# Optimization experiments

Measured on AMD Instinct MI355X. Metric: run time of the kernel, lower is better.

The kernel has to match this reference:

```python
import jax, jax.numpy as jnp
import numpy as np

B, NLOC, F, H = 16384, 12, 512, 256

def setup_inputs() -> dict:
    key = jax.random.key(0)
    ks = jax.random.split(key, 8)
    s = lambda n: 1.0 / np.sqrt(n)
    return {
        "global_feature": jax.random.normal(ks[0], (B, F), jnp.float32),
        "local_features": jax.random.normal(ks[1], (B, NLOC, F), jnp.float32),
        "Wq": jax.random.normal(ks[2], (F, H), jnp.float32) * s(F),
        "bq": jnp.zeros((H,), jnp.float32),
        "Wk": jax.random.normal(ks[3], (F, H), jnp.float32) * s(F),
        "bk": jnp.zeros((H,), jnp.float32),
        "Wv": jax.random.normal(ks[4], (F, H), jnp.float32) * s(F),
        "bv": jnp.zeros((H,), jnp.float32),
        "w_dr": jax.random.normal(ks[5], (NLOC,), jnp.float32) * s(NLOC),  # Linear(12,1) weight
        "b_dr": jnp.zeros((), jnp.float32),
        "Wf": jax.random.normal(ks[6], (2 * H, F), jnp.float32) * s(2 * H),
        "bf": jnp.zeros((F,), jnp.float32),
    }

def reference(global_feature, local_features, Wq, bq, Wk, bk, Wv, bv, w_dr, b_dr, Wf, bf):
    scale = 1.0 / jnp.sqrt(jnp.float32(H))
    # dimension_reduction over the 12 local tokens: Linear(12 -> 1)
    lf_mean = jnp.einsum('bkf,k->bf', local_features, w_dr) + b_dr  # [B, F]
    # --- local queries attend to the single global token ---
    gk = global_feature @ Wk + bk                       # [B, H]
    gv = global_feature @ Wv + bv                       # [B, H]
    lq = local_features @ Wq + bq                       # [B, 12, H]
    s1 = (jnp.einsum('bkh,bh->bk', lq, gk) * scale)[..., None]  # [B, 12, 1]
    a1 = jax.nn.softmax(s1, axis=-1)                    # softmax over length-1 key axis
    weighted_global = a1 * gv[:, None, :]               # [B, 12, H]
    # --- global query attends over the 12 local tokens ---
    gq = global_feature @ Wq + bq                       # [B, H]
    lk = local_features @ Wk + bk                       # [B, 12, H]
    lv = local_features @ Wv + bv                       # [B, 12, H]
    s2 = jnp.einsum('bh,bkh->bk', gq, lk) * scale       # [B, 12]
    a2 = jax.nn.softmax(s2, axis=-1)
    local_to_global = jnp.einsum('bk,bkh->bh', a2, lv)  # [B, H]
    # pool the 12-token axis of the weighted global feature
    wg_mean = jnp.einsum('bkh,k->bh', weighted_global, w_dr) + b_dr  # [B, H]
    combined = jnp.concatenate([local_to_global, wg_mean], axis=-1)  # [B, 2H]
    fused = jax.nn.relu(combined @ Wf + bf) + lf_mean + global_feature  # [B, F]
    return fused
```

## Files before the change

### kernel.cpp

```cpp
#include <hip/hip_runtime.h>

#define NLOC 12
#define F_DIM 512
#define H_DIM 256

typedef float f4 __attribute__((ext_vector_type(4)));
typedef _Float16 half4 __attribute__((ext_vector_type(4)));
typedef _Float16 half8 __attribute__((ext_vector_type(8)));

#define OFF_W1   0ul
#define OFF_W2   (OFF_W1 + 512ul*512*2)
#define OFF_C1   (OFF_W2 + 512ul*1024*2)
#define OFF_CVEC (OFF_C1 + 2048ul)
#define OFF_ACAT (OFF_CVEC + 2048ul)
#define OFF_BASE (OFF_ACAT + 16384ul*1024*2)

__global__ void __launch_bounds__(256) precompute_w(
    const float* __restrict__ Wq, const float* __restrict__ Wk,
    const float* __restrict__ Wv, const float* __restrict__ Wf,
    const float* __restrict__ wdr,
    _Float16* __restrict__ W1, _Float16* __restrict__ W2)
{
    __shared__ float X[32][264];
    __shared__ float Y[32][264];
    const int mode = blockIdx.z;
    const int f0 = blockIdx.x * 32;
    const int j0 = blockIdx.y * 32;
    const int t = threadIdx.x;

    {
        const int r = t >> 3, cb = (t & 7) * 32;
        const float* ysrc = ((mode == 0) ? Wq : Wv) + (j0 + r) * H_DIM + cb;
#pragma unroll
        for (int u = 0; u < 32; u += 4)
            *(f4*)&Y[r][cb + u] = *(const f4*)(ysrc + u);
        if (mode == 0) {
            const float* xsrc = Wk + (f0 + r) * H_DIM + cb;
#pragma unroll
            for (int u = 0; u < 32; u += 4)
                *(f4*)&X[r][cb + u] = *(const f4*)(xsrc + u);
        }
    }
    if (mode != 0) {
        const int h = t;
        const int hoff = (mode == 2) ? H_DIM : 0;
        const float* xsrc = Wf + (long)(h + hoff) * F_DIM + f0;
        f4 v[8];
#pragma unroll
        for (int u = 0; u < 8; ++u) v[u] = *(const f4*)(xsrc + u * 4);
#pragma unroll
        for (int r = 0; r < 32; ++r) X[r][h] = v[r >> 2][r & 3];
    }
    __syncthreads();

    const int fy = t >> 4, jx = t & 15;
    float a00 = 0.f, a01 = 0.f, a10 = 0.f, a11 = 0.f;
#pragma unroll 8
    for (int h = 0; h < H_DIM; ++h) {
        float x0 = X[fy][h], x1 = X[fy + 16][h];
        float y0 = Y[jx][h], y1 = Y[jx + 16][h];
        a00 += x0 * y0; a01 += x0 * y1; a10 += x1 * y0; a11 += x1 * y1;
    }
    if (mode == 2) {
        float S = 0.f;
#pragma unroll
        for (int k = 0; k < NLOC; ++k) S += wdr[k];
        a00 *= S; a01 *= S; a10 *= S; a11 *= S;
    }
    if (mode == 0) {
        W1[(f0 + fy) * F_DIM + (j0 + jx)]             = (_Float16)a00;
        W1[(f0 + fy) * F_DIM + (j0 + jx + 16)]        = (_Float16)a01;
        W1[(f0 + fy + 16) * F_DIM + (j0 + jx)]        = (_Float16)a10;
        W1[(f0 + fy + 16) * F_DIM + (j0 + jx + 16)]   = (_Float16)a11;
    } else {
        const long co = (mode == 2) ? F_DIM : 0;
        W2[(long)(f0 + fy) * 1024 + co + (j0 + jx)]           = (_Float16)a00;
        W2[(long)(f0 + fy) * 1024 + co + (j0 + jx + 16)]      = (_Float16)a01;
        W2[(long)(f0 + fy + 16) * 1024 + co + (j0 + jx)]      = (_Float16)a10;
        W2[(long)(f0 + fy + 16) * 1024 + co + (j0 + jx + 16)] = (_Float16)a11;
    }
}

__global__ void __launch_bounds__(256) cvec_kernel(
    const float* __restrict__ Wk, const float* __restrict__ Wf,
    const float* __restrict__ bq, const float* __restrict__ bv,
    const float* __restrict__ wdr, const float* __restrict__ bdr,
    const float* __restrict__ bfv,
    float* __restrict__ c1, float* __restrict__ cvec)
{
    const int f = blockIdx.x * 256 + threadIdx.x;
    f4 a = {0.f, 0.f, 0.f, 0.f};
    const f4* wk4 = (const f4*)(Wk + (long)f * H_DIM);
    const f4* bq4 = (const f4*)bq;
#pragma unroll 4
    for (int h4 = 0; h4 < H_DIM / 4; ++h4) a += wk4[h4] * bq4[h4];
    c1[f] = a[0] + a[1] + a[2] + a[3];

    float s1 = 0.f, s2 = 0.f, s3 = 0.f;
#pragma unroll 4
    for (int h = 0; h < H_DIM; ++h) {
        float w1v = Wf[h * F_DIM + f];
        float w2v = Wf[(H_DIM + h) * F_DIM + f];
        float bvh = bv[h];
        s1 += bvh * w1v; s2 += bvh * w2v; s3 += w2v;
    }
    float S = 0.f;
#pragma unroll
    for (int k = 0; k < NLOC; ++k) S += wdr[k];
    cvec[f] = s1 + S * s2 + bdr[0] * s3 + bfv[f];
}

__global__ void __launch_bounds__(256, 2) fused_local(
    const float* __restrict__ g, const float* __restrict__ loc,
    const _Float16* __restrict__ W1, const float* __restrict__ c1,
    const float* __restrict__ wdr, const float* __restrict__ bdr,
    _Float16* __restrict__ Acat, _Float16* __restrict__ base)
{
    __shared__ _Float16 G[32][520];
    __shared__ _Float16 T[32][520];
    const int tid = threadIdx.x;
    const int lane = tid & 63;
    const int wave = tid >> 6;
    const int quad = lane >> 4;
    const int l16 = lane & 15;
    const long m0 = (long)blockIdx.x * 32;

    {
        const int r = tid >> 3;
        const int cb = (tid & 7) * 8;
#pragma unroll
        for (int u = 0; u < 512; u += 64) {
            const float* src = g + (m0 + r) * F_DIM + cb + u;
            f4 v0 = *(const f4*)(src);
            f4 v1 = *(const f4*)(src + 4);
            half8 hv;
#pragma unroll
            for (int j = 0; j < 4; ++j) { hv[j] = (_Float16)v0[j]; hv[4 + j] = (_Float16)v1[j]; }
            *(half8*)&G[r][cb + u] = hv;
            *(half8*)(Acat + (m0 + r) * 1024 + 512 + cb + u) = hv;
        }
    }
    __syncthreads();

    const int wn1 = wave * 32;
    for (int nt = 0; nt < 4; ++nt) {
        const int n0 = nt * 128;
        const _Float16* wb0 = W1 + (long)(n0 + wn1 + l16) * F_DIM + quad * 8;
        const _Float16* wb1 = wb0 + 16 * F_DIM;
        f4 acc[2][2] = {{{0.f,0.f,0.f,0.f},{0.f,0.f,0.f,0.f}},
                        {{0.f,0.f,0.f,0.f},{0.f,0.f,0.f,0.f}}};
#pragma unroll
        for (int k0 = 0; k0 < 512; k0 += 32) {
            half8 b0 = *(const half8*)(wb0 + k0);
            half8 b1 = *(const half8*)(wb1 + k0);
            half8 a0 = *(const half8*)&G[l16][k0 + quad * 8];
            half8 a1 = *(const half8*)&G[16 + l16][k0 + quad * 8];
            acc[0][0] = __builtin_amdgcn_mfma_f32_16x16x32_f16(a0, b0, acc[0][0], 0, 0, 0);
            acc[0][1] = __builtin_amdgcn_mfma_f32_16x16x32_f16(a0, b1, acc[0][1], 0, 0, 0);
            acc[1][0] = __builtin_amdgcn_mfma_f32_16x16x32_f16(a1, b0, acc[1][0], 0, 0, 0);
            acc[1][1] = __builtin_amdgcn_mfma_f32_16x16x32_f16(a1, b1, acc[1][1], 0, 0, 0);
        }
#pragma unroll
        for (int ni = 0; ni < 2; ++ni) {
            const int col = n0 + wn1 + ni * 16 + l16;
            const float cv = c1[col];
#pragma unroll
            for (int mi = 0; mi < 2; ++mi)
#pragma unroll
                for (int i = 0; i < 4; ++i)
                    T[mi * 16 + quad * 4 + i][col] = (_Float16)(acc[mi][ni][i] + cv);
        }
    }
    __syncthreads();

    const int c0 = lane * 4;
    const int c1i = 256 + lane * 4;
    const float bd = bdr[0];
    float wv[NLOC];
#pragma unroll
    for (int k = 0; k < NLOC; ++k) wv[k] = wdr[k];

    for (int rr = 0; rr < 8; ++rr) {
        const int bl = wave * 8 + rr;
        const long b = m0 + bl;
        const float* lb = loc + b * (NLOC * F_DIM);

        f4 la[NLOC], lbv[NLOC];
#pragma unroll
        for (int k = 0; k < NLOC; ++k) {
            la[k]  = *(const f4*)(lb + k * F_DIM + c0);
            lbv[k] = *(const f4*)(lb + k * F_DIM + c1i);
        }
        f4 taf = __builtin_convertvector(*(const half4*)&T[bl][c0], f4);
        f4 tbf = __builtin_convertvector(*(const half4*)&T[bl][c1i], f4);

        float p[NLOC];
#pragma unroll
        for (int k = 0; k < NLOC; ++k) {
            f4 prod = la[k] * taf + lbv[k] * tbf;
            p[k] = prod[0] + prod[1] + prod[2] + prod[3];
        }
#pragma unroll
        for (int k = 0; k < NLOC; ++k) {
            float v = p[k];
            v += __shfl_xor(v, 1);
            v += __shfl_xor(v, 2);
            v += __shfl_xor(v, 4);
            v += __shfl_xor(v, 8);
            v += __shfl_xor(v, 16);
            v += __shfl_xor(v, 32);
            p[k] = v * 0.0625f;
        }
        float mx = p[0];
#pragma unroll
        for (int k = 1; k < NLOC; ++k) mx = fmaxf(mx, p[k]);
        float e[NLOC], s = 0.f;
#pragma unroll
        for (int k = 0; k < NLOC; ++k) { e[k] = expf(p[k] - mx); s += e[k]; }
        const float inv = 1.f / s;

        f4 pA = {0.f,0.f,0.f,0.f}, pB = {0.f,0.f,0.f,0.f};
        f4 fA = {0.f,0.f,0.f,0.f}, fB = {0.f,0.f,0.f,0.f};
#pragma unroll
        for (int k = 0; k < NLOC; ++k) {
            const float ak = e[k] * inv;
            const float wk = wv[k];
            pA += ak * la[k]; pB += ak * lbv[k];
            fA += wk * la[k]; fB += wk * lbv[k];
        }
        half4 gA = *(const half4*)&G[bl][c0];
        half4 gB = *(const half4*)&G[bl][c1i];
        fA += bd + __builtin_convertvector(gA, f4);
        fB += bd + __builtin_convertvector(gB, f4);

        *(half4*)(Acat + b * 1024 + c0)          = __builtin_convertvector(pA, half4);
        *(half4*)(Acat + b * 1024 + c1i)         = __builtin_convertvector(pB, half4);
        *(half4*)(base + b * F_DIM + c0)         = __builtin_convertvector(fA, half4);
        *(half4*)(base + b * F_DIM + c1i)        = __builtin_convertvector(fB, half4);
    }
}

__global__ void __launch_bounds__(256, 3) gemm_final(
    const _Float16* __restrict__ A, const _Float16* __restrict__ Bt,
    const float* __restrict__ cvec, const _Float16* __restrict__ base,
    float* __restrict__ out)
{
    __shared__ _Float16 As[2][64][40];
    const int tid = threadIdx.x;
    const int lane = tid & 63;
    const int wave = tid >> 6;
    const int quad = lane >> 4;
    const int l16 = lane & 15;
    const int wm = (wave & 1) * 32;
    const int wn = (wave >> 1) * 64;
    const long m0 = (long)blockIdx.x * 64;
    const int n0 = blockIdx.y * 128;
    const int srA = tid >> 2, scA = (tid & 3) * 8;

    const _Float16* bp0 = Bt + (long)(n0 + wn + l16) * 1024 + quad * 8;
    const _Float16* bp1 = bp0 + 16 * 1024;
    const _Float16* bp2 = bp0 + 32 * 1024;
    const _Float16* bp3 = bp0 + 48 * 1024;
    const _Float16* ap  = A + (m0 + srA) * 1024 + scA;

    f4 acc[2][4];
#pragma unroll
    for (int mi = 0; mi < 2; ++mi)
#pragma unroll
        for (int nj = 0; nj < 4; ++nj) acc[mi][nj] = (f4){0.f,0.f,0.f,0.f};

    *(uint4*)&As[0][srA][scA] = *(const uint4*)(ap);
    __syncthreads();

#pragma unroll
    for (int kt = 0; kt < 32; ++kt) {
        const int k0 = kt * 32;
        uint4 avn;
        if (kt < 31) avn = *(const uint4*)(ap + k0 + 32);
        half8 b0 = *(const half8*)(bp0 + k0);
        half8 b1 = *(const half8*)(bp1 + k0);
        half8 b2 = *(const half8*)(bp2 + k0);
        half8 b3 = *(const half8*)(bp3 + k0);
        half8 a0 = *(const half8*)&As[kt & 1][wm + l16][quad * 8];
        half8 a1 = *(const half8*)&As[kt & 1][wm + 16 + l16][quad * 8];
        acc[0][0] = __builtin_amdgcn_mfma_f32_16x16x32_f16(a0, b0, acc[0][0], 0, 0, 0);
        acc[1][0] = __builtin_amdgcn_mfma_f32_16x16x32_f16(a1, b0, acc[1][0], 0, 0, 0);
        acc[0][1] = __builtin_amdgcn_mfma_f32_16x16x32_f16(a0, b1, acc[0][1], 0, 0, 0);
        acc[1][1] = __builtin_amdgcn_mfma_f32_16x16x32_f16(a1, b1, acc[1][1], 0, 0, 0);
        acc[0][2] = __builtin_amdgcn_mfma_f32_16x16x32_f16(a0, b2, acc[0][2], 0, 0, 0);
        acc[1][2] = __builtin_amdgcn_mfma_f32_16x16x32_f16(a1, b2, acc[1][2], 0, 0, 0);
        acc[0][3] = __builtin_amdgcn_mfma_f32_16x16x32_f16(a0, b3, acc[0][3], 0, 0, 0);
        acc[1][3] = __builtin_amdgcn_mfma_f32_16x16x32_f16(a1, b3, acc[1][3], 0, 0, 0);
        if (kt < 31) *(uint4*)&As[(kt & 1) ^ 1][srA][scA] = avn;
        __syncthreads();
    }

#pragma unroll
    for (int mi = 0; mi < 2; ++mi)
#pragma unroll
        for (int nj = 0; nj < 4; ++nj) {
            const int col = n0 + wn + nj * 16 + l16;
            const float cv = cvec[col];
#pragma unroll
            for (int i = 0; i < 4; ++i) {
                const long row = m0 + wm + mi * 16 + quad * 4 + i;
                float v = acc[mi][nj][i] + cv;
                v = fmaxf(v, 0.f) + (float)base[row * F_DIM + col];
                out[row * F_DIM + col] = v;
            }
        }
}

extern "C" void kernel_launch(void* const* d_in, const int* in_sizes, int n_in,
                              void* d_out, int out_size, void* d_ws, size_t ws_size,
                              hipStream_t stream)
{
    (void)in_sizes; (void)n_in; (void)out_size; (void)ws_size;
    const float* gf  = (const float*)d_in[0];
    const float* loc = (const float*)d_in[1];
    const float* Wq  = (const float*)d_in[2];
    const float* bq  = (const float*)d_in[3];
    const float* Wk  = (const float*)d_in[4];
    const float* Wv  = (const float*)d_in[6];
    const float* bv  = (const float*)d_in[7];
    const float* wdr = (const float*)d_in[8];
    const float* bdr = (const float*)d_in[9];
    const float* Wf  = (const float*)d_in[10];
    const float* bfv = (const float*)d_in[11];
    float* out = (float*)d_out;

    char* ws = (char*)d_ws;
    _Float16* W1   = (_Float16*)(ws + OFF_W1);
    _Float16* W2   = (_Float16*)(ws + OFF_W2);
    float*    c1   = (float*)(ws + OFF_C1);
    float*    cvec = (float*)(ws + OFF_CVEC);
    _Float16* Acat = (_Float16*)(ws + OFF_ACAT);
    _Float16* base = (_Float16*)(ws + OFF_BASE);

    precompute_w<<<dim3(16, 16, 3), 256, 0, stream>>>(Wq, Wk, Wv, Wf, wdr, W1, W2);
    cvec_kernel<<<2, 256, 0, stream>>>(Wk, Wf, bq, bv, wdr, bdr, bfv, c1, cvec);
    fused_local<<<512, 256, 0, stream>>>(gf, loc, W1, c1, wdr, bdr, Acat, base);
    gemm_final<<<dim3(256, 4), 256, 0, stream>>>(Acat, W2, cvec, base, out);
}
```

Baseline: 719.7 us.

## Enlarge final GEMM tile with LDS-staged B, prefetch local rows, merge cvec kernel

The final GEMM moves from 64x128 to 128x128 block tiles. Both A and B are now staged through double-buffered shared memory, and each wave computes a 4x4 grid of MFMA tiles, which raises reuse and cuts redundant global B loads. The fused_local kernel now software-pipelines the next row's first half of local features during the current row's compute, and its barrier moves after the first prefetch. The cvec kernel is folded into precompute_w as an extra grid slice to save one launch. The larger tile uses more registers and LDS, so launch bounds drop to 2 blocks per SM and grid-level parallelism is halved.

```diff
diff --git a/kernel.cpp b/kernel.cpp
--- a/kernel.cpp
+++ b/kernel.cpp
@@ -18,15 +18,44 @@
 __global__ void __launch_bounds__(256) precompute_w(
     const float* __restrict__ Wq, const float* __restrict__ Wk,
     const float* __restrict__ Wv, const float* __restrict__ Wf,
-    const float* __restrict__ wdr,
-    _Float16* __restrict__ W1, _Float16* __restrict__ W2)
+    const float* __restrict__ wdr, const float* __restrict__ bq,
+    const float* __restrict__ bv, const float* __restrict__ bdr,
+    const float* __restrict__ bfv,
+    _Float16* __restrict__ W1, _Float16* __restrict__ W2,
+    float* __restrict__ c1, float* __restrict__ cvec)
 {
+    const int mode = blockIdx.z;
+    const int t = threadIdx.x;
+
+    if (mode == 3) {
+        if (blockIdx.y != 0 || blockIdx.x >= 2) return;
+        const int f = blockIdx.x * 256 + t;
+        f4 a = {0.f, 0.f, 0.f, 0.f};
+        const f4* wk4 = (const f4*)(Wk + (long)f * H_DIM);
+        const f4* bq4 = (const f4*)bq;
+#pragma unroll 4
+        for (int h4 = 0; h4 < H_DIM / 4; ++h4) a += wk4[h4] * bq4[h4];
+        c1[f] = a[0] + a[1] + a[2] + a[3];
+
+        float s1 = 0.f, s2 = 0.f, s3 = 0.f;
+#pragma unroll 4
+        for (int h = 0; h < H_DIM; ++h) {
+            float w1v = Wf[h * F_DIM + f];
+            float w2v = Wf[(H_DIM + h) * F_DIM + f];
+            float bvh = bv[h];
+            s1 += bvh * w1v; s2 += bvh * w2v; s3 += w2v;
+        }
+        float S = 0.f;
+#pragma unroll
+        for (int k = 0; k < NLOC; ++k) S += wdr[k];
+        cvec[f] = s1 + S * s2 + bdr[0] * s3 + bfv[f];
+        return;
+    }
+
     __shared__ float X[32][264];
     __shared__ float Y[32][264];
-    const int mode = blockIdx.z;
     const int f0 = blockIdx.x * 32;
     const int j0 = blockIdx.y * 32;
-    const int t = threadIdx.x;
 
     {
         const int r = t >> 3, cb = (t & 7) * 32;
@@ -79,35 +108,6 @@
         W2[(long)(f0 + fy + 16) * 1024 + co + (j0 + jx)]      = (_Float16)a10;
         W2[(long)(f0 + fy + 16) * 1024 + co + (j0 + jx + 16)] = (_Float16)a11;
     }
-}
-
-__global__ void __launch_bounds__(256) cvec_kernel(
-    const float* __restrict__ Wk, const float* __restrict__ Wf,
-    const float* __restrict__ bq, const float* __restrict__ bv,
-    const float* __restrict__ wdr, const float* __restrict__ bdr,
-    const float* __restrict__ bfv,
-    float* __restrict__ c1, float* __restrict__ cvec)
-{
-    const int f = blockIdx.x * 256 + threadIdx.x;
-    f4 a = {0.f, 0.f, 0.f, 0.f};
-    const f4* wk4 = (const f4*)(Wk + (long)f * H_DIM);
-    const f4* bq4 = (const f4*)bq;
-#pragma unroll 4
-    for (int h4 = 0; h4 < H_DIM / 4; ++h4) a += wk4[h4] * bq4[h4];
-    c1[f] = a[0] + a[1] + a[2] + a[3];
-
-    float s1 = 0.f, s2 = 0.f, s3 = 0.f;
-#pragma unroll 4
-    for (int h = 0; h < H_DIM; ++h) {
-        float w1v = Wf[h * F_DIM + f];
-        float w2v = Wf[(H_DIM + h) * F_DIM + f];
-        float bvh = bv[h];
-        s1 += bvh * w1v; s2 += bvh * w2v; s3 += w2v;
-    }
-    float S = 0.f;
-#pragma unroll
-    for (int k = 0; k < NLOC; ++k) S += wdr[k];
-    cvec[f] = s1 + S * s2 + bdr[0] * s3 + bfv[f];
 }
 
 __global__ void __launch_bounds__(256, 2) fused_local(
@@ -171,7 +171,6 @@
                     T[mi * 16 + quad * 4 + i][col] = (_Float16)(acc[mi][ni][i] + cv);
         }
     }
-    __syncthreads();
 
     const int c0 = lane * 4;
     const int c1i = 256 + lane * 4;
@@ -180,17 +179,30 @@
 #pragma unroll
     for (int k = 0; k < NLOC; ++k) wv[k] = wdr[k];
 
-    for (int rr = 0; rr < 8; ++rr) {
+    f4 laA[NLOC], laB[NLOC];
+    {
+        const float* lb0 = loc + (m0 + wave * 8) * (NLOC * F_DIM);
+#pragma unroll
+        for (int k = 0; k < NLOC; ++k) laA[k] = *(const f4*)(lb0 + k * F_DIM + c0);
+    }
+    __syncthreads();
+
+    auto row_body = [&](int rr, f4 (&la)[NLOC], f4 (&laN)[NLOC]) {
         const int bl = wave * 8 + rr;
         const long b = m0 + bl;
         const float* lb = loc + b * (NLOC * F_DIM);
 
-        f4 la[NLOC], lbv[NLOC];
-#pragma unroll
-        for (int k = 0; k < NLOC; ++k) {
-            la[k]  = *(const f4*)(lb + k * F_DIM + c0);
+        f4 lbv[NLOC];
+#pragma unroll
+        for (int k = 0; k < NLOC; ++k)
             lbv[k] = *(const f4*)(lb + k * F_DIM + c1i);
-        }
+        if (rr < 7) {
+            const float* lbn = lb + NLOC * F_DIM;
+#pragma unroll
+            for (int k = 0; k < NLOC; ++k)
+                laN[k] = *(const f4*)(lbn + k * F_DIM + c0);
+        }
+
         f4 taf = __builtin_convertvector(*(const half4*)&T[bl][c0], f4);
         f4 tbf = __builtin_convertvector(*(const half4*)&T[bl][c1i], f4);
 
@@ -237,66 +249,87 @@
         *(half4*)(Acat + b * 1024 + c1i)         = __builtin_convertvector(pB, half4);
         *(half4*)(base + b * F_DIM + c0)         = __builtin_convertvector(fA, half4);
         *(half4*)(base + b * F_DIM + c1i)        = __builtin_convertvector(fB, half4);
+    };
+
+#pragma unroll
+    for (int it = 0; it < 4; ++it) {
+        row_body(it * 2,     laA, laB);
+        row_body(it * 2 + 1, laB, laA);
     }
 }
 
-__global__ void __launch_bounds__(256, 3) gemm_final(
+__global__ void __launch_bounds__(256, 2) gemm_final(
     const _Float16* __restrict__ A, const _Float16* __restrict__ Bt,
     const float* __restrict__ cvec, const _Float16* __restrict__ base,
     float* __restrict__ out)
 {
-    __shared__ _Float16 As[2][64][40];
+    __shared__ _Float16 As[2][128][40];
+    __shared__ _Float16 Bs[2][128][40];
     const int tid = threadIdx.x;
     const int lane = tid & 63;
     const int wave = tid >> 6;
     const int quad = lane >> 4;
     const int l16 = lane & 15;
-    const int wm = (wave & 1) * 32;
+    const int wm = (wave & 1) * 64;
     const int wn = (wave >> 1) * 64;
-    const long m0 = (long)blockIdx.x * 64;
+    const long m0 = (long)blockIdx.x * 128;
     const int n0 = blockIdx.y * 128;
-    const int srA = tid >> 2, scA = (tid & 3) * 8;
-
-    const _Float16* bp0 = Bt + (long)(n0 + wn + l16) * 1024 + quad * 8;
-    const _Float16* bp1 = bp0 + 16 * 1024;
-    const _Float16* bp2 = bp0 + 32 * 1024;
-    const _Float16* bp3 = bp0 + 48 * 1024;
-    const _Float16* ap  = A + (m0 + srA) * 1024 + scA;
-
-    f4 acc[2][4];
-#pragma unroll
-    for (int mi = 0; mi < 2; ++mi)
+    const int sr = tid >> 1, sc = (tid & 1) * 16;
+
+    const _Float16* ap = A  + (m0 + sr) * 1024 + sc;
+    const _Float16* bp = Bt + (long)(n0 + sr) * 1024 + sc;
+
+    f4 acc[4][4];
+#pragma unroll
+    for (int mi = 0; mi < 4; ++mi)
 #pragma unroll
         for (int nj = 0; nj < 4; ++nj) acc[mi][nj] = (f4){0.f,0.f,0.f,0.f};
 
-    *(uint4*)&As[0][srA][scA] = *(const uint4*)(ap);
+    {
+        uint4 a0 = *(const uint4*)(ap);
+        uint4 a1 = *(const uint4*)(ap + 8);
+        uint4 b0 = *(const uint4*)(bp);
+        uint4 b1 = *(const uint4*)(bp + 8);
+        *(uint4*)&As[0][sr][sc]     = a0;
+        *(uint4*)&As[0][sr][sc + 8] = a1;
+        *(uint4*)&Bs[0][sr][sc]     = b0;
+        *(uint4*)&Bs[0][sr][sc + 8] = b1;
+    }
     __syncthreads();
 
-#pragma unroll
+#pragma unroll 4
     for (int kt = 0; kt < 32; ++kt) {
-        const int k0 = kt * 32;
-        uint4 avn;
-        if (kt < 31) avn = *(const uint4*)(ap + k0 + 32);
-        half8 b0 = *(const half8*)(bp0 + k0);
-        half8 b1 = *(const half8*)(bp1 + k0);
-        half8 b2 = *(const half8*)(bp2 + k0);
-        half8 b3 = *(const half8*)(bp3 + k0);
-        half8 a0 = *(const half8*)&As[kt & 1][wm + l16][quad * 8];
-        half8 a1 = *(const half8*)&As[kt & 1][wm + 16 + l16][quad * 8];
-        acc[0][0] = __builtin_amdgcn_mfma_f32_16x16x32_f16(a0, b0, acc[0][0], 0, 0, 0);
-        acc[1][0] = __builtin_amdgcn_mfma_f32_16x16x32_f16(a1, b0, acc[1][0], 0, 0, 0);
-        acc[0][1] = __builtin_amdgcn_mfma_f32_16x16x32_f16(a0, b1, acc[0][1], 0, 0, 0);
-        acc[1][1] = __builtin_amdgcn_mfma_f32_16x16x32_f16(a1, b1, acc[1][1], 0, 0, 0);
-        acc[0][2] = __builtin_amdgcn_mfma_f32_16x16x32_f16(a0, b2, acc[0][2], 0, 0, 0);
-        acc[1][2] = __builtin_amdgcn_mfma_f32_16x16x32_f16(a1, b2, acc[1][2], 0, 0, 0);
-        acc[0][3] = __builtin_amdgcn_mfma_f32_16x16x32_f16(a0, b3, acc[0][3], 0, 0, 0);
-        acc[1][3] = __builtin_amdgcn_mfma_f32_16x16x32_f16(a1, b3, acc[1][3], 0, 0, 0);
-        if (kt < 31) *(uint4*)&As[(kt & 1) ^ 1][srA][scA] = avn;
+        const int cur = kt & 1;
+        uint4 a0, a1, b0, b1;
+        if (kt < 31) {
+            const int k0 = (kt + 1) * 32;
+            a0 = *(const uint4*)(ap + k0);
+            a1 = *(const uint4*)(ap + k0 + 8);
+            b0 = *(const uint4*)(bp + k0);
+            b1 = *(const uint4*)(bp + k0 + 8);
+        }
+        half8 af[4], bf[4];
+#pragma unroll
+        for (int i = 0; i < 4; ++i) {
+            af[i] = *(const half8*)&As[cur][wm + i * 16 + l16][quad * 8];
+            bf[i] = *(const half8*)&Bs[cur][wn + i * 16 + l16][quad * 8];
+        }
+#pragma unroll
+        for (int mi = 0; mi < 4; ++mi)
+#pragma unroll
+            for (int nj = 0; nj < 4; ++nj)
+                acc[mi][nj] = __builtin_amdgcn_mfma_f32_16x16x32_f16(af[mi], bf[nj], acc[mi][nj], 0, 0, 0);
+        if (kt < 31) {
+            *(uint4*)&As[cur ^ 1][sr][sc]     = a0;
+            *(uint4*)&As[cur ^ 1][sr][sc + 8] = a1;
+            *(uint4*)&Bs[cur ^ 1][sr][sc]     = b0;
+            *(uint4*)&Bs[cur ^ 1][sr][sc + 8] = b1;
+        }
         __syncthreads();
     }
 
 #pragma unroll
-    for (int mi = 0; mi < 2; ++mi)
+    for (int mi = 0; mi < 4; ++mi)
 #pragma unroll
         for (int nj = 0; nj < 4; ++nj) {
             const int col = n0 + wn + nj * 16 + l16;
@@ -337,8 +370,8 @@
     _Float16* Acat = (_Float16*)(ws + OFF_ACAT);
     _Float16* base = (_Float16*)(ws + OFF_BASE);
 
-    precompute_w<<<dim3(16, 16, 3), 256, 0, stream>>>(Wq, Wk, Wv, Wf, wdr, W1, W2);
-    cvec_kernel<<<2, 256, 0, stream>>>(Wk, Wf, bq, bv, wdr, bdr, bfv, c1, cvec);
+    precompute_w<<<dim3(16, 16, 4), 256, 0, stream>>>(
+        Wq, Wk, Wv, Wf, wdr, bq, bv, bdr, bfv, W1, W2, c1, cvec);
     fused_local<<<512, 256, 0, stream>>>(gf, loc, W1, c1, wdr, bdr, Acat, base);
-    gemm_final<<<dim3(256, 4), 256, 0, stream>>>(Acat, W2, cvec, base, out);
+    gemm_final<<<dim3(128, 4), 256, 0, stream>>>(Acat, W2, cvec, base, out);
 }
```

New measurement: 679.5 us. -5.6%, faster.
